# Performance work log

Measured on AMD Instinct MI355X. Metric: run time of the kernel, lower is better.

Reference implementation:

```python
import jax, jax.numpy as jnp
import numpy as np

N_NODES = 100000
N_EDGES = 1600000


def gcn_conv(x, W, b, src, dst, ew, n):
    """PyG GCNConv: x@W, symmetric deg^-1/2 norm with self-loops, scatter-add at dst, +b."""
    loop = jnp.arange(n, dtype=src.dtype)
    s = jnp.concatenate([src, loop])            # sources incl. self-loops
    d = jnp.concatenate([dst, loop])            # targets incl. self-loops
    w = jnp.concatenate([ew, jnp.ones((n,), ew.dtype)])  # self-loop weight = 1
    deg = jax.ops.segment_sum(w, d, num_segments=n)      # weighted in-degree
    dinv = jnp.where(deg > 0, jax.lax.rsqrt(deg), 0.0)
    norm = dinv[s] * w * dinv[d]                # [E+N]
    h = x @ W                                   # [N, F_out]
    msg = h[s] * norm[:, None]                  # gather + per-edge scale
    out = jax.ops.segment_sum(msg, d, num_segments=n)    # scatter-add
    return out + b


def setup_inputs() -> dict:
    key = jax.random.key(0)
    ks = jax.random.split(key, 8)
    in_dim, hid, lat = 128, 128, 64
    x = jax.random.normal(ks[0], (N_NODES, in_dim), jnp.float32)
    edge_index = jax.random.randint(ks[1], (2, N_EDGES), 0, N_NODES, dtype=jnp.int32)
    weights = jax.random.uniform(ks[2], (N_EDGES,), jnp.float32)
    s_in = 1.0 / np.sqrt(in_dim)
    s_h = 1.0 / np.sqrt(hid)
    return {
        "x": x,
        "edge_index": edge_index,
        "weights": weights,
        "W1": jax.random.normal(ks[3], (in_dim, hid), jnp.float32) * s_in,
        "b1": jnp.zeros((hid,), jnp.float32),
        "W2": jax.random.normal(ks[4], (hid, hid), jnp.float32) * s_h,
        "b2": jnp.zeros((hid,), jnp.float32),
        "W_mu": jax.random.normal(ks[5], (hid, lat), jnp.float32) * s_h,
        "b_mu": jnp.zeros((lat,), jnp.float32),
        "W_lv": jax.random.normal(ks[6], (hid, lat), jnp.float32) * s_h,
        "b_lv": jnp.zeros((lat,), jnp.float32),
    }


def reference(x, edge_index, weights, W1, b1, W2, b2, W_mu, b_mu, W_lv, b_lv):
    n = x.shape[0]
    src, dst = edge_index[0], edge_index[1]
    h = jax.nn.relu(gcn_conv(x, W1, b1, src, dst, weights, n))
    h = gcn_conv(h, W2, b2, src, dst, weights, n)
    g = jnp.mean(h, axis=0, keepdims=True)      # [1, hid] global mean pool
    mu = g @ W_mu + b_mu
    logvar = g @ W_lv + b_lv
    return (mu, logvar)
```

## Files before the change

### kernel.cpp

```cpp
#include <hip/hip_runtime.h>


typedef __bf16 bf16x8 __attribute__((ext_vector_type(8)));
typedef float f32x4 __attribute__((ext_vector_type(4)));
typedef float f32x2 __attribute__((ext_vector_type(2)));
typedef unsigned long long u64;

#define RE   2048
#define BSH  8
#define BCAP 5120
#define NBMX 392

__device__ __forceinline__ float bf2f(unsigned short u){
  return __uint_as_float(((unsigned)u) << 16);
}
__device__ __forceinline__ unsigned short f2bf(float f){
  unsigned u = __float_as_uint(f);
  u += 0x7fffu + ((u >> 16) & 1u);
  return (unsigned short)(u >> 16);
}
__device__ __forceinline__ __bf16 us2bf(unsigned short u){
  __bf16 b; __builtin_memcpy(&b, &u, 2); return b;
}
__device__ __forceinline__ float ldf(const void* p, int i, int isf32){
  return isf32 ? ((const float*)p)[i] : bf2f(((const unsigned short*)p)[i]);
}
__device__ __forceinline__ void fma8f8(float* acc, float n, uint2 h){
  f32x2 p0 = __builtin_amdgcn_cvt_pk_f32_fp8((int)h.x, false);
  f32x2 p1 = __builtin_amdgcn_cvt_pk_f32_fp8((int)h.x, true);
  f32x2 p2 = __builtin_amdgcn_cvt_pk_f32_fp8((int)h.y, false);
  f32x2 p3 = __builtin_amdgcn_cvt_pk_f32_fp8((int)h.y, true);
  acc[0] = fmaf(n, p0[0], acc[0]);
  acc[1] = fmaf(n, p0[1], acc[1]);
  acc[2] = fmaf(n, p1[0], acc[2]);
  acc[3] = fmaf(n, p1[1], acc[3]);
  acc[4] = fmaf(n, p2[0], acc[4]);
  acc[5] = fmaf(n, p2[1], acc[5]);
  acc[6] = fmaf(n, p3[0], acc[6]);
  acc[7] = fmaf(n, p3[1], acc[7]);
}

__device__ __forceinline__ void scanBuckets(int* __restrict__ cnt, int* __restrict__ sm,
    int* __restrict__ hrow, int* __restrict__ rrow, int NB, int tid){
  const int K = (NBMX + 255) / 256;
  int c0 = tid * K;
  int loc = 0;
  #pragma unroll
  for (int i = 0; i < K; ++i){
    int j = c0 + i;
    if (j < NB) loc += cnt[j];
  }
  sm[tid] = loc;
  __syncthreads();
  for (int off = 1; off < 256; off <<= 1){
    int tmp = (tid >= off) ? sm[tid - off] : 0;
    __syncthreads();
    sm[tid] += tmp;
    __syncthreads();
  }
  int running = sm[tid] - loc;
  #pragma unroll
  for (int i = 0; i < K; ++i){
    int j = c0 + i;
    if (j < NB){
      int old = cnt[j];
      hrow[j] = old;
      rrow[j] = running;
      cnt[j] = running;
      running += old;
    }
  }
}

__global__ void k_init(const unsigned* __restrict__ xw, int* __restrict__ flag,
                       const void* __restrict__ W1, unsigned short* __restrict__ W1T,
                       float* __restrict__ v){
  __shared__ int s[256];
  int t = threadIdx.x;
  int cnt = 0;
  for (int k = t; k < 4096; k += 256){
    unsigned lo = xw[k] & 0xFFFFu;
    int e = (int)((lo >> 7) & 0xFFu);
    if ((e >= 100 && e <= 141) || (lo & 0x7FFFu) == 0) cnt++;
  }
  s[t] = cnt;
  __syncthreads();
  for (int off = 128; off > 0; off >>= 1){
    if (t < off) s[t] += s[t + off];
    __syncthreads();
  }
  int isf32 = (s[0] < 2458) ? 1 : 0;
  if (blockIdx.x == 0){
    if (t == 0) *flag = isf32;
    if (t < 128) v[t] = 0.0f;
  }
  int gid = blockIdx.x * 256 + t;
  int k = gid & 127, n = gid >> 7;
  W1T[gid] = isf32 ? f2bf(((const float*)W1)[k * 128 + n])
                   : ((const unsigned short*)W1)[k * 128 + n];
}

__global__ void __launch_bounds__(256) k_bin(const int* __restrict__ src,
    const int* __restrict__ dst, const void* __restrict__ w,
    u64* __restrict__ stagD, u64* __restrict__ stagS,
    int* __restrict__ histD, int* __restrict__ roffD,
    int* __restrict__ histS, int* __restrict__ roffS,
    int E, int NB, const int* __restrict__ flagp){
  __shared__ int cntD[NBMX];
  __shared__ int cntS[NBMX];
  __shared__ u64 stag[RE];
  __shared__ int sm[256];
  int tid = threadIdx.x;
  int r = blockIdx.x;
  for (int i = tid; i < NB; i += 256){ cntD[i] = 0; cntS[i] = 0; }
  __syncthreads();
  int isf32 = *flagp;
  int e0 = r * RE;
  int en = E - e0; if (en > RE) en = RE;
  u64 rec[8];
  #pragma unroll
  for (int k = 0; k < 8; ++k){
    int o = k * 256 + tid;
    rec[k] = ~0ull;
    if (o < en){
      int idx = e0 + o;
      int s_ = src[idx], d_ = dst[idx];
      float wf = ldf(w, idx, isf32);
      int wq = (int)(wf * 32768.0f + 0.5f);
      if (wq > 32767) wq = 32767;
      rec[k] = ((u64)(unsigned)d_ << 32) | ((u64)(unsigned)s_ << 15) | (unsigned)wq;
      atomicAdd(&cntD[d_ >> BSH], 1);
      atomicAdd(&cntS[s_ >> BSH], 1);
    }
  }
  __syncthreads();
  scanBuckets(cntD, sm, histD + (size_t)r * NB, roffD + (size_t)r * NB, NB, tid);
  __syncthreads();
  #pragma unroll
  for (int k = 0; k < 8; ++k){
    if (rec[k] != ~0ull){
      int p = atomicAdd(&cntD[(int)(rec[k] >> 32) >> BSH], 1);
      stag[p] = rec[k];
    }
  }
  __syncthreads();
  u64* opD = stagD + (size_t)r * RE;
  for (int i = tid; i < en; i += 256) opD[i] = stag[i];
  __syncthreads();
  scanBuckets(cntS, sm, histS + (size_t)r * NB, roffS + (size_t)r * NB, NB, tid);
  __syncthreads();
  #pragma unroll
  for (int k = 0; k < 8; ++k){
    if (rec[k] != ~0ull){
      int d_ = (int)(rec[k] >> 32);
      int s_ = (int)((rec[k] >> 15) & 0x1FFFFu);
      unsigned wq = (unsigned)(rec[k] & 32767u);
      u64 rs = ((u64)(unsigned)s_ << 32) | ((u64)(unsigned)d_ << 15) | wq;
      int p = atomicAdd(&cntS[s_ >> BSH], 1);
      stag[p] = rs;
    }
  }
  __syncthreads();
  u64* opS = stagS + (size_t)r * RE;
  for (int i = tid; i < en; i += 256) opS[i] = stag[i];
}

__global__ void __launch_bounds__(256) k_transp4(const int* __restrict__ A,
    const int* __restrict__ B, const int* __restrict__ C, const int* __restrict__ D,
    int* __restrict__ AT, int* __restrict__ BT, int* __restrict__ CT,
    int* __restrict__ DT, int NR, int NB){
  __shared__ int ta[32][33];
  __shared__ int tb[32][33];
  __shared__ int tc[32][33];
  __shared__ int td[32][33];
  int bx = (int)blockIdx.x * 32;
  int by = (int)blockIdx.y * 32;
  int tx = threadIdx.x & 31, ty = threadIdx.x >> 5;
  for (int yy = ty; yy < 32; yy += 8){
    int r = by + yy, b = bx + tx;
    int v1 = 0, v2 = 0, v3 = 0, v4 = 0;
    if (r < NR && b < NB){
      size_t o = (size_t)r * NB + b;
      v1 = A[o]; v2 = B[o]; v3 = C[o]; v4 = D[o];
    }
    ta[yy][tx] = v1; tb[yy][tx] = v2; tc[yy][tx] = v3; td[yy][tx] = v4;
  }
  __syncthreads();
  for (int yy = ty; yy < 32; yy += 8){
    int b = bx + yy, r = by + tx;
    if (b < NB && r < NR){
      size_t o = (size_t)b * NR + r;
      AT[o] = ta[tx][yy]; BT[o] = tb[tx][yy];
      CT[o] = tc[tx][yy]; DT[o] = td[tx][yy];
    }
  }
}

__global__ void __launch_bounds__(512) k_fold(const u64* __restrict__ stagD,
    const int* __restrict__ histT, const int* __restrict__ roffT,
    float* __restrict__ dinv, int2* __restrict__ rc,
    unsigned* __restrict__ edges, int NR, int N){
  __shared__ unsigned cd[256];
  __shared__ float dinvL[256];
  __shared__ int cur[256];
  __shared__ int sm[256];
  __shared__ unsigned recs[BCAP];
  int b = blockIdx.x, tid = threadIdx.x;
  int lo = b << BSH;
  int nn = N - lo; if (nn > 256) nn = 256;
  if (tid < 256) cd[tid] = 0u;
  __syncthreads();
  const int* hrow = histT + (size_t)b * NR;
  const int* rrow = roffT + (size_t)b * NR;
  for (int r = tid; r < NR; r += 512){
    int len = hrow[r];
    if (len == 0) continue;
    const u64* rp = stagD + (size_t)r * RE + rrow[r];
    for (int k = 0; k < len; ++k){
      u64 rec = rp[k];
      int dl = (int)(rec >> 32) - lo;
      atomicAdd(&cd[dl], (1u << 20) | (unsigned)((rec & 32767u) >> 2));
    }
  }
  __syncthreads();
  int c = 0;
  if (tid < 256){
    unsigned p = cd[tid];
    float di = rsqrtf(1.0f + (float)(p & 0xFFFFFu) * (1.0f / 8192.0f));
    dinvL[tid] = di;
    c = (int)(p >> 20);
    if (tid < nn) dinv[lo + tid] = di;
    sm[tid] = c;
  }
  __syncthreads();
  for (int off = 1; off < 256; off <<= 1){
    int tmp = (tid < 256 && tid >= off) ? sm[tid - off] : 0;
    __syncthreads();
    if (tid < 256) sm[tid] += tmp;
    __syncthreads();
  }
  if (tid < 256){
    int pre = sm[tid] - c;
    cur[tid] = pre;
    if (tid < nn) rc[lo + tid] = make_int2(b * BCAP + pre, c);
  }
  __syncthreads();
  int tot = sm[255];
  for (int r = tid; r < NR; r += 512){
    int len = hrow[r];
    if (len == 0) continue;
    const u64* rp = stagD + (size_t)r * RE + rrow[r];
    for (int k = 0; k < len; ++k){
      u64 rec = rp[k];
      int dl = (int)(rec >> 32) - lo;
      int s_ = (int)((rec >> 15) & 0x1FFFFu);
      int wq = (int)(rec & 32767u);
      int nq = (int)((float)wq * dinvL[dl] + 0.5f);
      if (nq > 32767) nq = 32767;
      int p = atomicAdd(&cur[dl], 1);
      if (p < BCAP) recs[p] = ((unsigned)s_ << 15) | (unsigned)nq;
    }
  }
  __syncthreads();
  if (tid < 16 && tot + tid < BCAP) recs[tot + tid] = 0u;
  __syncthreads();
  int lim = tot + 16; if (lim > BCAP) lim = BCAP;
  unsigned* op = edges + (size_t)b * BCAP;
  for (int i = tid; i < lim; i += 512) op[i] = recs[i];
}

__global__ void __launch_bounds__(256) k_postG(const void* __restrict__ xv,
    const __bf16* __restrict__ wt, unsigned char* __restrict__ H,
    const u64* __restrict__ stagS, const int* __restrict__ histST,
    const int* __restrict__ roffST, const float* __restrict__ dinv,
    float2* __restrict__ dc, int nbg, int NR, int N,
    const int* __restrict__ flagp){
  __shared__ float SL[256];
  int tid = threadIdx.x;
  if ((int)blockIdx.x < nbg){
    int wave = ((int)blockIdx.x * 256 + tid) >> 6;
    int lane = tid & 63;
    int row16 = wave << 4;
    if (row16 >= N) return;
    int isf32 = *flagp;
    int m = lane & 15, q = lane >> 4;
    bf16x8 a0, a1, a2, a3;
    if (isf32){
      const float* ap = (const float*)xv + (size_t)(row16 + m) * 128 + q * 8;
      #pragma unroll
      for (int j = 0; j < 8; ++j){
        a0[j] = us2bf(f2bf(ap[j +  0]));
        a1[j] = us2bf(f2bf(ap[j + 32]));
        a2[j] = us2bf(f2bf(ap[j + 64]));
        a3[j] = us2bf(f2bf(ap[j + 96]));
      }
    } else {
      const __bf16* ap = (const __bf16*)xv + (size_t)(row16 + m) * 128 + q * 8;
      a0 = *(const bf16x8*)(ap +  0);
      a1 = *(const bf16x8*)(ap + 32);
      a2 = *(const bf16x8*)(ap + 64);
      a3 = *(const bf16x8*)(ap + 96);
    }
    float4 dv = *(const float4*)(dinv + row16 + q * 4);
    for (int nt = 0; nt < 8; ++nt){
      const __bf16* bp = wt + (size_t)(nt * 16 + m) * 128 + q * 8;
      bf16x8 b0 = *(const bf16x8*)(bp +  0);
      bf16x8 b1 = *(const bf16x8*)(bp + 32);
      bf16x8 b2 = *(const bf16x8*)(bp + 64);
      bf16x8 b3 = *(const bf16x8*)(bp + 96);
      f32x4 acc = {0.f, 0.f, 0.f, 0.f};
      acc = __builtin_amdgcn_mfma_f32_16x16x32_bf16(a0, b0, acc, 0, 0, 0);
      acc = __builtin_amdgcn_mfma_f32_16x16x32_bf16(a1, b1, acc, 0, 0, 0);
      acc = __builtin_amdgcn_mfma_f32_16x16x32_bf16(a2, b2, acc, 0, 0, 0);
      acc = __builtin_amdgcn_mfma_f32_16x16x32_bf16(a3, b3, acc, 0, 0, 0);
      unsigned char* op = H + (size_t)(row16 + q * 4) * 128 + nt * 16 + m;
      float v0 = acc[0] * dv.x, v1 = acc[1] * dv.y;
      float v2 = acc[2] * dv.z, v3 = acc[3] * dv.w;
      op[0]   = (unsigned char)(__builtin_amdgcn_cvt_pk_fp8_f32(v0, v0, 0, false) & 0xFF);
      op[128] = (unsigned char)(__builtin_amdgcn_cvt_pk_fp8_f32(v1, v1, 0, false) & 0xFF);
      op[256] = (unsigned char)(__builtin_amdgcn_cvt_pk_fp8_f32(v2, v2, 0, false) & 0xFF);
      op[384] = (unsigned char)(__builtin_amdgcn_cvt_pk_fp8_f32(v3, v3, 0, false) & 0xFF);
    }
    return;
  }
  int b = (int)blockIdx.x - nbg;
  int lo = b << BSH;
  int nn = N - lo; if (nn > 256) nn = 256;
  if (tid < 256) SL[tid] = 0.0f;
  __syncthreads();
  const int* hrow = histST + (size_t)b * NR;
  const int* rrow = roffST + (size_t)b * NR;
  for (int r = tid; r < NR; r += 256){
    int len = hrow[r];
    if (len == 0) continue;
    const u64* rp = stagS + (size_t)r * RE + rrow[r];
    for (int k = 0; k < len; ++k){
      u64 rec = rp[k];
      int s_ = (int)(rec >> 32);
      int d_ = (int)((rec >> 15) & 0x1FFFFu);
      float wqf = (float)(rec & 32767u) * (1.0f / 32768.0f);
      atomicAdd(&SL[s_ - lo], wqf * dinv[d_]);
    }
  }
  __syncthreads();
  if (tid < nn){
    int i = lo + tid;
    float di = dinv[i];
    dc[i] = make_float2(di, di * di + di * SL[tid]);
  }
}

__global__ void __launch_bounds__(256) k_agg(const unsigned char* __restrict__ H,
    const int2* __restrict__ rc, const float2* __restrict__ dc,
    const unsigned* __restrict__ edges, const void* __restrict__ b1,
    float* __restrict__ v, int N, int totslots, const int* __restrict__ flagp){
  __shared__ float vsh[128];
  __shared__ float bsh[128];
  int tid = threadIdx.x;
  int isf32 = *flagp;
  if (tid < 128){ vsh[tid] = 0.0f; bsh[tid] = ldf(b1, tid, isf32); }
  __syncthreads();
  int lane = tid & 63;
  int wv = tid >> 6;
  int slot = lane >> 3;
  int q = lane & 7;
  const unsigned char* Hq = H + q * 16;
  float ax[16];
  #pragma unroll
  for (int j = 0; j < 16; ++j) ax[j] = 0.0f;
  int d = ((int)blockIdx.x * 4 + wv) * 8 + slot;
  int2 rcv = make_int2(0, 0); float2 dcv = make_float2(0.f, 0.f);
  uint4 hs = make_uint4(0u, 0u, 0u, 0u);
  if (d < N){
    rcv = rc[d]; dcv = dc[d];
    hs = *(const uint4*)(Hq + (size_t)d * 128);
  }
  while (d < N){
    int dn = d + totslots;
    int2 rcn = make_int2(0, 0); float2 dcn = make_float2(0.f, 0.f);
    uint4 hsn = make_uint4(0u, 0u, 0u, 0u);
    if (dn < N){
      rcn = rc[dn]; dcn = dc[dn];
      hsn = *(const uint4*)(Hq + (size_t)dn * 128);
    }
    float acc[16];
    #pragma unroll
    for (int j = 0; j < 16; ++j) acc[j] = 0.0f;
    fma8f8(acc,     dcv.x, make_uint2(hs.x, hs.y));
    fma8f8(acc + 8, dcv.x, make_uint2(hs.z, hs.w));
    int start = rcv.x, len = rcv.y;
    if (len > 0){
      const unsigned* ep = edges + start;
      unsigned e0 = ep[0], e1 = ep[1], e2 = ep[2], e3 = ep[3];
      uint4 h0 = *(const uint4*)(Hq + (size_t)(e0 >> 15) * 128);
      uint4 h1 = *(const uint4*)(Hq + (size_t)(e1 >> 15) * 128);
      uint4 h2 = *(const uint4*)(Hq + (size_t)(e2 >> 15) * 128);
      #pragma unroll 2
      for (int k = 0; k < len; ++k){
        unsigned en = ep[k + 4];
        uint4 hn = *(const uint4*)(Hq + (size_t)(e3 >> 15) * 128);
        float wn = (float)(e0 & 32767u) * (1.0f / 32768.0f);
        fma8f8(acc,     wn, make_uint2(h0.x, h0.y));
        fma8f8(acc + 8, wn, make_uint2(h0.z, h0.w));
        e0 = e1; e1 = e2; e2 = e3; e3 = en;
        h0 = h1; h1 = h2; h2 = hn;
      }
    }
    #pragma unroll
    for (int j = 0; j < 16; ++j){
      float rj = fmaxf(acc[j] + bsh[q * 16 + j], 0.0f);
      ax[j] = fmaf(dcv.y, rj, ax[j]);
    }
    d = dn; rcv = rcn; dcv = dcn; hs = hsn;
  }
  #pragma unroll
  for (int j = 0; j < 16; ++j){
    ax[j] += __shfl_xor(ax[j], 8);
    ax[j] += __shfl_xor(ax[j], 16);
    ax[j] += __shfl_xor(ax[j], 32);
  }
  if (slot == 0){
    #pragma unroll
    for (int j = 0; j < 16; ++j) atomicAdd(&vsh[q * 16 + j], ax[j]);
  }
  __syncthreads();
  if (tid < 128) atomicAdd(&v[tid], vsh[tid]);
}

__global__ void __launch_bounds__(128) k_head(const float* __restrict__ v,
    const void* __restrict__ W2, const void* __restrict__ b2,
    const void* __restrict__ Wmu, const void* __restrict__ bmu,
    const void* __restrict__ Wlv, const void* __restrict__ blv,
    void* __restrict__ outv, float invN, const int* __restrict__ flagp){
  __shared__ float gsh[128];
  __shared__ float tsh[128];
  int t = threadIdx.x;
  int isf32 = *flagp;
  gsh[t] = v[t] * invN;
  __syncthreads();
  float acc = ldf(b2, t, isf32);
  for (int k = 0; k < 128; ++k) acc = fmaf(gsh[k], ldf(W2, k * 128 + t, isf32), acc);
  tsh[t] = acc;
  __syncthreads();
  int j = t & 63;
  const void* Wp = (t < 64) ? Wmu : Wlv;
  float o = ldf((t < 64) ? bmu : blv, j, isf32);
  for (int k = 0; k < 128; ++k) o = fmaf(tsh[k], ldf(Wp, k * 64 + j, isf32), o);
  if (isf32) ((float*)outv)[t] = o;
  else       ((unsigned short*)outv)[t] = f2bf(o);
}

extern "C" void kernel_launch(void* const* d_in, const int* in_sizes, int n_in,
                              void* d_out, int out_size, void* d_ws, size_t ws_size,
                              hipStream_t stream) {
  const void* x   = d_in[0];
  const int*  ei  = (const int*)d_in[1];
  const void* w   = d_in[2];
  const void* W1  = d_in[3];
  const void* b1  = d_in[4];
  const void* W2  = d_in[5];
  const void* b2  = d_in[6];
  const void* Wmu = d_in[7];
  const void* bmu = d_in[8];
  const void* Wlv = d_in[9];
  const void* blv = d_in[10];

  const int N = in_sizes[0] / 128;
  const int E = in_sizes[2];
  const int* src = ei;
  const int* dst = ei + E;

  char* wsb = (char*)d_ws;
  size_t off = 0;
  auto alloc = [&](size_t bytes) -> void* {
    off = (off + 255) & ~(size_t)255;
    void* p = wsb + off;
    off += bytes;
    return p;
  };
  const int NR  = (E + RE - 1) / RE;
  const int NB  = (N + 255) >> BSH;
  int*   flag     = (int*)  alloc(16);
  float* dinv     = (float*)alloc((size_t)N * 4 + 16);
  float2* dc      = (float2*)alloc((size_t)N * 8);
  int2*   rc      = (int2*) alloc((size_t)N * 8);
  float* v        = (float*)alloc(128 * 4);
  unsigned short* W1T = (unsigned short*)alloc(128 * 128 * 2);
  u64*   stagD    = (u64*)  alloc((size_t)NR * RE * 8);
  u64*   stagS    = (u64*)  alloc((size_t)NR * RE * 8);
  int*   histD    = (int*)  alloc((size_t)NR * NB * 4);
  int*   roffD    = (int*)  alloc((size_t)NR * NB * 4);
  int*   histS    = (int*)  alloc((size_t)NR * NB * 4);
  int*   roffS    = (int*)  alloc((size_t)NR * NB * 4);
  int*   histDT   = (int*)  alloc((size_t)NB * NR * 4);
  int*   roffDT   = (int*)  alloc((size_t)NB * NR * 4);
  int*   histST   = (int*)  alloc((size_t)NB * NR * 4);
  int*   roffST   = (int*)  alloc((size_t)NB * NR * 4);
  unsigned* edges = (unsigned*)alloc((size_t)NB * BCAP * 4 + 64);
  unsigned char* H = (unsigned char*)alloc((size_t)N * 128);
  (void)ws_size; (void)n_in; (void)out_size;

  const int nwaves = (N + 15) / 16;
  const int nb_g = (nwaves + 3) / 4;

  k_init<<<64, 256, 0, stream>>>((const unsigned*)x, flag, W1, W1T, v);
  k_bin<<<NR, 256, 0, stream>>>(src, dst, w, stagD, stagS,
                                histD, roffD, histS, roffS, E, NB, flag);
  dim3 tg((NB + 31) / 32, (NR + 31) / 32);
  k_transp4<<<tg, 256, 0, stream>>>(histD, roffD, histS, roffS,
                                    histDT, roffDT, histST, roffST, NR, NB);
  k_fold<<<NB, 512, 0, stream>>>(stagD, histDT, roffDT, dinv, rc, edges, NR, N);
  k_postG<<<nb_g + NB, 256, 0, stream>>>(x, (const __bf16*)W1T, H,
                                         stagS, histST, roffST, dinv, dc,
                                         nb_g, NR, N, flag);
  const int nb_agg = 1024;
  k_agg<<<nb_agg, 256, 0, stream>>>(H, rc, dc, edges, b1, v, N, nb_agg * 32, flag);
  k_head<<<1, 128, 0, stream>>>(v, W2, b2, Wmu, bmu, Wlv, blv,
                                d_out, 1.0f / (float)N, flag);
}
```

Baseline: 300.8 us.

## Overlap the feature GEMM with edge binning and split the fold stage

The x@W1 MFMA GEMM now runs in extra blocks of the binning kernel, so it no longer waits for degree normalisation. Because of that, H is stored unscaled and the full symmetric norm dinv[s]*w*dinv[d] goes into each quantised edge record instead. The old fold kernel is split in two. k_foldA computes only degrees and row counts. k_post2 then fills the per-bucket edge lists and the self-loop/dc terms in parallel blocks. This shortens the dependent chain and spreads work over more blocks, at the cost of one extra launch, a second pass over the staged edges, and more dinv gathers per edge.

```diff
diff --git a/kernel.cpp b/kernel.cpp
--- a/kernel.cpp
+++ b/kernel.cpp
@@ -100,185 +100,22 @@
                    : ((const unsigned short*)W1)[k * 128 + n];
 }
 
-__global__ void __launch_bounds__(256) k_bin(const int* __restrict__ src,
+__global__ void __launch_bounds__(256) k_binG(const int* __restrict__ src,
     const int* __restrict__ dst, const void* __restrict__ w,
     u64* __restrict__ stagD, u64* __restrict__ stagS,
     int* __restrict__ histD, int* __restrict__ roffD,
     int* __restrict__ histS, int* __restrict__ roffS,
-    int E, int NB, const int* __restrict__ flagp){
+    int E, int NB, int NR,
+    const void* __restrict__ xv, const __bf16* __restrict__ wt,
+    unsigned char* __restrict__ H, int N, const int* __restrict__ flagp){
   __shared__ int cntD[NBMX];
   __shared__ int cntS[NBMX];
   __shared__ u64 stag[RE];
   __shared__ int sm[256];
   int tid = threadIdx.x;
-  int r = blockIdx.x;
-  for (int i = tid; i < NB; i += 256){ cntD[i] = 0; cntS[i] = 0; }
-  __syncthreads();
-  int isf32 = *flagp;
-  int e0 = r * RE;
-  int en = E - e0; if (en > RE) en = RE;
-  u64 rec[8];
-  #pragma unroll
-  for (int k = 0; k < 8; ++k){
-    int o = k * 256 + tid;
-    rec[k] = ~0ull;
-    if (o < en){
-      int idx = e0 + o;
-      int s_ = src[idx], d_ = dst[idx];
-      float wf = ldf(w, idx, isf32);
-      int wq = (int)(wf * 32768.0f + 0.5f);
-      if (wq > 32767) wq = 32767;
-      rec[k] = ((u64)(unsigned)d_ << 32) | ((u64)(unsigned)s_ << 15) | (unsigned)wq;
-      atomicAdd(&cntD[d_ >> BSH], 1);
-      atomicAdd(&cntS[s_ >> BSH], 1);
-    }
-  }
-  __syncthreads();
-  scanBuckets(cntD, sm, histD + (size_t)r * NB, roffD + (size_t)r * NB, NB, tid);
-  __syncthreads();
-  #pragma unroll
-  for (int k = 0; k < 8; ++k){
-    if (rec[k] != ~0ull){
-      int p = atomicAdd(&cntD[(int)(rec[k] >> 32) >> BSH], 1);
-      stag[p] = rec[k];
-    }
-  }
-  __syncthreads();
-  u64* opD = stagD + (size_t)r * RE;
-  for (int i = tid; i < en; i += 256) opD[i] = stag[i];
-  __syncthreads();
-  scanBuckets(cntS, sm, histS + (size_t)r * NB, roffS + (size_t)r * NB, NB, tid);
-  __syncthreads();
-  #pragma unroll
-  for (int k = 0; k < 8; ++k){
-    if (rec[k] != ~0ull){
-      int d_ = (int)(rec[k] >> 32);
-      int s_ = (int)((rec[k] >> 15) & 0x1FFFFu);
-      unsigned wq = (unsigned)(rec[k] & 32767u);
-      u64 rs = ((u64)(unsigned)s_ << 32) | ((u64)(unsigned)d_ << 15) | wq;
-      int p = atomicAdd(&cntS[s_ >> BSH], 1);
-      stag[p] = rs;
-    }
-  }
-  __syncthreads();
-  u64* opS = stagS + (size_t)r * RE;
-  for (int i = tid; i < en; i += 256) opS[i] = stag[i];
-}
-
-__global__ void __launch_bounds__(256) k_transp4(const int* __restrict__ A,
-    const int* __restrict__ B, const int* __restrict__ C, const int* __restrict__ D,
-    int* __restrict__ AT, int* __restrict__ BT, int* __restrict__ CT,
-    int* __restrict__ DT, int NR, int NB){
-  __shared__ int ta[32][33];
-  __shared__ int tb[32][33];
-  __shared__ int tc[32][33];
-  __shared__ int td[32][33];
-  int bx = (int)blockIdx.x * 32;
-  int by = (int)blockIdx.y * 32;
-  int tx = threadIdx.x & 31, ty = threadIdx.x >> 5;
-  for (int yy = ty; yy < 32; yy += 8){
-    int r = by + yy, b = bx + tx;
-    int v1 = 0, v2 = 0, v3 = 0, v4 = 0;
-    if (r < NR && b < NB){
-      size_t o = (size_t)r * NB + b;
-      v1 = A[o]; v2 = B[o]; v3 = C[o]; v4 = D[o];
-    }
-    ta[yy][tx] = v1; tb[yy][tx] = v2; tc[yy][tx] = v3; td[yy][tx] = v4;
-  }
-  __syncthreads();
-  for (int yy = ty; yy < 32; yy += 8){
-    int b = bx + yy, r = by + tx;
-    if (b < NB && r < NR){
-      size_t o = (size_t)b * NR + r;
-      AT[o] = ta[tx][yy]; BT[o] = tb[tx][yy];
-      CT[o] = tc[tx][yy]; DT[o] = td[tx][yy];
-    }
-  }
-}
-
-__global__ void __launch_bounds__(512) k_fold(const u64* __restrict__ stagD,
-    const int* __restrict__ histT, const int* __restrict__ roffT,
-    float* __restrict__ dinv, int2* __restrict__ rc,
-    unsigned* __restrict__ edges, int NR, int N){
-  __shared__ unsigned cd[256];
-  __shared__ float dinvL[256];
-  __shared__ int cur[256];
-  __shared__ int sm[256];
-  __shared__ unsigned recs[BCAP];
-  int b = blockIdx.x, tid = threadIdx.x;
-  int lo = b << BSH;
-  int nn = N - lo; if (nn > 256) nn = 256;
-  if (tid < 256) cd[tid] = 0u;
-  __syncthreads();
-  const int* hrow = histT + (size_t)b * NR;
-  const int* rrow = roffT + (size_t)b * NR;
-  for (int r = tid; r < NR; r += 512){
-    int len = hrow[r];
-    if (len == 0) continue;
-    const u64* rp = stagD + (size_t)r * RE + rrow[r];
-    for (int k = 0; k < len; ++k){
-      u64 rec = rp[k];
-      int dl = (int)(rec >> 32) - lo;
-      atomicAdd(&cd[dl], (1u << 20) | (unsigned)((rec & 32767u) >> 2));
-    }
-  }
-  __syncthreads();
-  int c = 0;
-  if (tid < 256){
-    unsigned p = cd[tid];
-    float di = rsqrtf(1.0f + (float)(p & 0xFFFFFu) * (1.0f / 8192.0f));
-    dinvL[tid] = di;
-    c = (int)(p >> 20);
-    if (tid < nn) dinv[lo + tid] = di;
-    sm[tid] = c;
-  }
-  __syncthreads();
-  for (int off = 1; off < 256; off <<= 1){
-    int tmp = (tid < 256 && tid >= off) ? sm[tid - off] : 0;
-    __syncthreads();
-    if (tid < 256) sm[tid] += tmp;
-    __syncthreads();
-  }
-  if (tid < 256){
-    int pre = sm[tid] - c;
-    cur[tid] = pre;
-    if (tid < nn) rc[lo + tid] = make_int2(b * BCAP + pre, c);
-  }
-  __syncthreads();
-  int tot = sm[255];
-  for (int r = tid; r < NR; r += 512){
-    int len = hrow[r];
-    if (len == 0) continue;
-    const u64* rp = stagD + (size_t)r * RE + rrow[r];
-    for (int k = 0; k < len; ++k){
-      u64 rec = rp[k];
-      int dl = (int)(rec >> 32) - lo;
-      int s_ = (int)((rec >> 15) & 0x1FFFFu);
-      int wq = (int)(rec & 32767u);
-      int nq = (int)((float)wq * dinvL[dl] + 0.5f);
-      if (nq > 32767) nq = 32767;
-      int p = atomicAdd(&cur[dl], 1);
-      if (p < BCAP) recs[p] = ((unsigned)s_ << 15) | (unsigned)nq;
-    }
-  }
-  __syncthreads();
-  if (tid < 16 && tot + tid < BCAP) recs[tot + tid] = 0u;
-  __syncthreads();
-  int lim = tot + 16; if (lim > BCAP) lim = BCAP;
-  unsigned* op = edges + (size_t)b * BCAP;
-  for (int i = tid; i < lim; i += 512) op[i] = recs[i];
-}
-
-__global__ void __launch_bounds__(256) k_postG(const void* __restrict__ xv,
-    const __bf16* __restrict__ wt, unsigned char* __restrict__ H,
-    const u64* __restrict__ stagS, const int* __restrict__ histST,
-    const int* __restrict__ roffST, const float* __restrict__ dinv,
-    float2* __restrict__ dc, int nbg, int NR, int N,
-    const int* __restrict__ flagp){
-  __shared__ float SL[256];
-  int tid = threadIdx.x;
-  if ((int)blockIdx.x < nbg){
-    int wave = ((int)blockIdx.x * 256 + tid) >> 6;
+  if ((int)blockIdx.x >= NR){
+    int gb = (int)blockIdx.x - NR;
+    int wave = (gb * 256 + tid) >> 6;
     int lane = tid & 63;
     int row16 = wave << 4;
     if (row16 >= N) return;
@@ -301,7 +138,6 @@
       a2 = *(const bf16x8*)(ap + 64);
       a3 = *(const bf16x8*)(ap + 96);
     }
-    float4 dv = *(const float4*)(dinv + row16 + q * 4);
     for (int nt = 0; nt < 8; ++nt){
       const __bf16* bp = wt + (size_t)(nt * 16 + m) * 128 + q * 8;
       bf16x8 b0 = *(const bf16x8*)(bp +  0);
@@ -314,40 +150,209 @@
       acc = __builtin_amdgcn_mfma_f32_16x16x32_bf16(a2, b2, acc, 0, 0, 0);
       acc = __builtin_amdgcn_mfma_f32_16x16x32_bf16(a3, b3, acc, 0, 0, 0);
       unsigned char* op = H + (size_t)(row16 + q * 4) * 128 + nt * 16 + m;
-      float v0 = acc[0] * dv.x, v1 = acc[1] * dv.y;
-      float v2 = acc[2] * dv.z, v3 = acc[3] * dv.w;
-      op[0]   = (unsigned char)(__builtin_amdgcn_cvt_pk_fp8_f32(v0, v0, 0, false) & 0xFF);
-      op[128] = (unsigned char)(__builtin_amdgcn_cvt_pk_fp8_f32(v1, v1, 0, false) & 0xFF);
-      op[256] = (unsigned char)(__builtin_amdgcn_cvt_pk_fp8_f32(v2, v2, 0, false) & 0xFF);
-      op[384] = (unsigned char)(__builtin_amdgcn_cvt_pk_fp8_f32(v3, v3, 0, false) & 0xFF);
+      op[0]   = (unsigned char)(__builtin_amdgcn_cvt_pk_fp8_f32(acc[0], acc[0], 0, false) & 0xFF);
+      op[128] = (unsigned char)(__builtin_amdgcn_cvt_pk_fp8_f32(acc[1], acc[1], 0, false) & 0xFF);
+      op[256] = (unsigned char)(__builtin_amdgcn_cvt_pk_fp8_f32(acc[2], acc[2], 0, false) & 0xFF);
+      op[384] = (unsigned char)(__builtin_amdgcn_cvt_pk_fp8_f32(acc[3], acc[3], 0, false) & 0xFF);
     }
     return;
   }
-  int b = (int)blockIdx.x - nbg;
+  int r = blockIdx.x;
+  for (int i = tid; i < NB; i += 256){ cntD[i] = 0; cntS[i] = 0; }
+  __syncthreads();
+  int isf32 = *flagp;
+  int e0 = r * RE;
+  int en = E - e0; if (en > RE) en = RE;
+  u64 rec[8];
+  #pragma unroll
+  for (int k = 0; k < 8; ++k){
+    int o = k * 256 + tid;
+    rec[k] = ~0ull;
+    if (o < en){
+      int idx = e0 + o;
+      int s_ = src[idx], d_ = dst[idx];
+      float wf = ldf(w, idx, isf32);
+      int wq = (int)(wf * 32768.0f + 0.5f);
+      if (wq > 32767) wq = 32767;
+      rec[k] = ((u64)(unsigned)d_ << 32) | ((u64)(unsigned)s_ << 15) | (unsigned)wq;
+      atomicAdd(&cntD[d_ >> BSH], 1);
+      atomicAdd(&cntS[s_ >> BSH], 1);
+    }
+  }
+  __syncthreads();
+  scanBuckets(cntD, sm, histD + (size_t)r * NB, roffD + (size_t)r * NB, NB, tid);
+  __syncthreads();
+  #pragma unroll
+  for (int k = 0; k < 8; ++k){
+    if (rec[k] != ~0ull){
+      int p = atomicAdd(&cntD[(int)(rec[k] >> 32) >> BSH], 1);
+      stag[p] = rec[k];
+    }
+  }
+  __syncthreads();
+  u64* opD = stagD + (size_t)r * RE;
+  for (int i = tid; i < en; i += 256) opD[i] = stag[i];
+  __syncthreads();
+  scanBuckets(cntS, sm, histS + (size_t)r * NB, roffS + (size_t)r * NB, NB, tid);
+  __syncthreads();
+  #pragma unroll
+  for (int k = 0; k < 8; ++k){
+    if (rec[k] != ~0ull){
+      int d_ = (int)(rec[k] >> 32);
+      int s_ = (int)((rec[k] >> 15) & 0x1FFFFu);
+      unsigned wq = (unsigned)(rec[k] & 32767u);
+      u64 rs = ((u64)(unsigned)s_ << 32) | ((u64)(unsigned)d_ << 15) | wq;
+      int p = atomicAdd(&cntS[s_ >> BSH], 1);
+      stag[p] = rs;
+    }
+  }
+  __syncthreads();
+  u64* opS = stagS + (size_t)NR * 0 + (size_t)r * RE;
+  opS = stagS + (size_t)r * RE;
+  for (int i = tid; i < en; i += 256) opS[i] = stag[i];
+}
+
+__global__ void __launch_bounds__(256) k_transp4(const int* __restrict__ A,
+    const int* __restrict__ B, const int* __restrict__ C, const int* __restrict__ D,
+    int* __restrict__ AT, int* __restrict__ BT, int* __restrict__ CT,
+    int* __restrict__ DT, int NR, int NB){
+  __shared__ int ta[32][33];
+  __shared__ int tb[32][33];
+  __shared__ int tc[32][33];
+  __shared__ int td[32][33];
+  int bx = (int)blockIdx.x * 32;
+  int by = (int)blockIdx.y * 32;
+  int tx = threadIdx.x & 31, ty = threadIdx.x >> 5;
+  for (int yy = ty; yy < 32; yy += 8){
+    int r = by + yy, b = bx + tx;
+    int v1 = 0, v2 = 0, v3 = 0, v4 = 0;
+    if (r < NR && b < NB){
+      size_t o = (size_t)r * NB + b;
+      v1 = A[o]; v2 = B[o]; v3 = C[o]; v4 = D[o];
+    }
+    ta[yy][tx] = v1; tb[yy][tx] = v2; tc[yy][tx] = v3; td[yy][tx] = v4;
+  }
+  __syncthreads();
+  for (int yy = ty; yy < 32; yy += 8){
+    int b = bx + yy, r = by + tx;
+    if (b < NB && r < NR){
+      size_t o = (size_t)b * NR + r;
+      AT[o] = ta[tx][yy]; BT[o] = tb[tx][yy];
+      CT[o] = tc[tx][yy]; DT[o] = td[tx][yy];
+    }
+  }
+}
+
+__global__ void __launch_bounds__(512) k_foldA(const u64* __restrict__ stagD,
+    const int* __restrict__ histT, const int* __restrict__ roffT,
+    float* __restrict__ dinv, int2* __restrict__ rc, int NR, int N){
+  __shared__ unsigned cd[256];
+  __shared__ int sm[256];
+  int b = blockIdx.x, tid = threadIdx.x;
   int lo = b << BSH;
   int nn = N - lo; if (nn > 256) nn = 256;
-  if (tid < 256) SL[tid] = 0.0f;
-  __syncthreads();
-  const int* hrow = histST + (size_t)b * NR;
-  const int* rrow = roffST + (size_t)b * NR;
-  for (int r = tid; r < NR; r += 256){
+  if (tid < 256) cd[tid] = 0u;
+  __syncthreads();
+  const int* hrow = histT + (size_t)b * NR;
+  const int* rrow = roffT + (size_t)b * NR;
+  for (int r = tid; r < NR; r += 512){
     int len = hrow[r];
     if (len == 0) continue;
-    const u64* rp = stagS + (size_t)r * RE + rrow[r];
+    const u64* rp = stagD + (size_t)r * RE + rrow[r];
     for (int k = 0; k < len; ++k){
       u64 rec = rp[k];
-      int s_ = (int)(rec >> 32);
-      int d_ = (int)((rec >> 15) & 0x1FFFFu);
-      float wqf = (float)(rec & 32767u) * (1.0f / 32768.0f);
-      atomicAdd(&SL[s_ - lo], wqf * dinv[d_]);
-    }
-  }
-  __syncthreads();
-  if (tid < nn){
-    int i = lo + tid;
-    float di = dinv[i];
-    dc[i] = make_float2(di, di * di + di * SL[tid]);
-  }
+      int dl = (int)(rec >> 32) - lo;
+      atomicAdd(&cd[dl], (1u << 20) | (unsigned)((rec & 32767u) >> 2));
+    }
+  }
+  __syncthreads();
+  int c = 0;
+  if (tid < 256){
+    unsigned p = cd[tid];
+    float di = rsqrtf(1.0f + (float)(p & 0xFFFFFu) * (1.0f / 8192.0f));
+    c = (int)(p >> 20);
+    if (tid < nn) dinv[lo + tid] = di;
+    sm[tid] = c;
+  }
+  __syncthreads();
+  for (int off = 1; off < 256; off <<= 1){
+    int tmp = (tid < 256 && tid >= off) ? sm[tid - off] : 0;
+    __syncthreads();
+    if (tid < 256) sm[tid] += tmp;
+    __syncthreads();
+  }
+  if (tid < nn) rc[lo + tid] = make_int2(b * BCAP + (sm[tid] - c), c);
+}
+
+__global__ void __launch_bounds__(512) k_post2(const u64* __restrict__ stagD,
+    const int* __restrict__ histDT, const int* __restrict__ roffDT,
+    const u64* __restrict__ stagS, const int* __restrict__ histST,
+    const int* __restrict__ roffST, const float* __restrict__ dinv,
+    const int2* __restrict__ rc, unsigned* __restrict__ edges,
+    float2* __restrict__ dc, int NR, int N){
+  __shared__ unsigned recs[BCAP];
+  __shared__ int cur[256];
+  int b = (int)blockIdx.x >> 1, tid = threadIdx.x;
+  int lo = b << BSH;
+  int nn = N - lo; if (nn > 256) nn = 256;
+  if (blockIdx.x & 1){
+    float* SL = (float*)recs;
+    if (tid < 256) SL[tid] = 0.0f;
+    __syncthreads();
+    const int* hrow = histST + (size_t)b * NR;
+    const int* rrow = roffST + (size_t)b * NR;
+    for (int r = tid; r < NR; r += 512){
+      int len = hrow[r];
+      if (len == 0) continue;
+      const u64* rp = stagS + (size_t)r * RE + rrow[r];
+      for (int k = 0; k < len; ++k){
+        u64 rec = rp[k];
+        int s_ = (int)(rec >> 32);
+        int d_ = (int)((rec >> 15) & 0x1FFFFu);
+        float wqf = (float)(rec & 32767u) * (1.0f / 32768.0f);
+        atomicAdd(&SL[s_ - lo], wqf * dinv[d_]);
+      }
+    }
+    __syncthreads();
+    if (tid < nn){
+      int i = lo + tid;
+      float di = dinv[i];
+      dc[i] = make_float2(di * di, di * di + di * SL[tid]);
+    }
+    return;
+  }
+  int tot = 0;
+  {
+    int2 last = rc[lo + nn - 1];
+    tot = (last.x - b * BCAP) + last.y;
+  }
+  if (tot > BCAP) tot = BCAP;
+  if (tid < nn) cur[tid] = rc[lo + tid].x - b * BCAP;
+  __syncthreads();
+  const int* hrow = histDT + (size_t)b * NR;
+  const int* rrow = roffDT + (size_t)b * NR;
+  for (int r = tid; r < NR; r += 512){
+    int len = hrow[r];
+    if (len == 0) continue;
+    const u64* rp = stagD + (size_t)r * RE + rrow[r];
+    for (int k = 0; k < len; ++k){
+      u64 rec = rp[k];
+      int d_ = (int)(rec >> 32);
+      int s_ = (int)((rec >> 15) & 0x1FFFFu);
+      int wq = (int)(rec & 32767u);
+      float nrm = dinv[s_] * ((float)wq * (1.0f / 32768.0f)) * dinv[d_];
+      int nq = (int)(nrm * 32768.0f + 0.5f);
+      if (nq > 32767) nq = 32767;
+      int p = atomicAdd(&cur[d_ - lo], 1);
+      if (p < BCAP) recs[p] = ((unsigned)s_ << 15) | (unsigned)nq;
+    }
+  }
+  __syncthreads();
+  if (tid < 16 && tot + tid < BCAP) recs[tot + tid] = 0u;
+  __syncthreads();
+  int lim = tot + 16; if (lim > BCAP) lim = BCAP;
+  unsigned* op = edges + (size_t)b * BCAP;
+  for (int i = tid; i < lim; i += 512) op[i] = recs[i];
 }
 
 __global__ void __launch_bounds__(256) k_agg(const unsigned char* __restrict__ H,
@@ -504,15 +509,15 @@
   const int nb_g = (nwaves + 3) / 4;
 
   k_init<<<64, 256, 0, stream>>>((const unsigned*)x, flag, W1, W1T, v);
-  k_bin<<<NR, 256, 0, stream>>>(src, dst, w, stagD, stagS,
-                                histD, roffD, histS, roffS, E, NB, flag);
+  k_binG<<<NR + nb_g, 256, 0, stream>>>(src, dst, w, stagD, stagS,
+                                        histD, roffD, histS, roffS, E, NB, NR,
+                                        x, (const __bf16*)W1T, H, N, flag);
   dim3 tg((NB + 31) / 32, (NR + 31) / 32);
   k_transp4<<<tg, 256, 0, stream>>>(histD, roffD, histS, roffS,
                                     histDT, roffDT, histST, roffST, NR, NB);
-  k_fold<<<NB, 512, 0, stream>>>(stagD, histDT, roffDT, dinv, rc, edges, NR, N);
-  k_postG<<<nb_g + NB, 256, 0, stream>>>(x, (const __bf16*)W1T, H,
-                                         stagS, histST, roffST, dinv, dc,
-                                         nb_g, NR, N, flag);
+  k_foldA<<<NB, 512, 0, stream>>>(stagD, histDT, roffDT, dinv, rc, NR, N);
+  k_post2<<<2 * NB, 512, 0, stream>>>(stagD, histDT, roffDT, stagS, histST,
+                                      roffST, dinv, rc, edges, dc, NR, N);
   const int nb_agg = 1024;
   k_agg<<<nb_agg, 256, 0, stream>>>(H, rc, dc, edges, b1, v, N, nb_agg * 32, flag);
   k_head<<<1, 128, 0, stream>>>(v, W2, b2, Wmu, bmu, Wlv, blv,
```

Measured after the change: 305.7 us. No clear change (+1.7%).
